# Kernel tuning notes

Hardware: AMD Instinct MI355X
Metric: run time of the kernel (lower is better)

Reference implementation:

```python
import jax, jax.numpy as jnp
import numpy as np
import math

N_HEAD = 16
N_KV_HEAD = 4
N_EMBED = 2048
HEAD_DIM = N_EMBED // N_HEAD  # 128
ROPE_BASE = 10000.0


def _rope_tables(T, dim, dtype):
    inv_freq = 1.0 / (ROPE_BASE ** (jnp.arange(0, dim, 2, dtype=jnp.float32) / dim))
    t = jnp.arange(T, dtype=jnp.float32)
    freqs = jnp.outer(t, inv_freq)            # (T, dim/2)
    emb = jnp.concatenate([freqs, freqs], -1) # (T, dim)
    return jnp.cos(emb).astype(dtype), jnp.sin(emb).astype(dtype)


def _rotate_half(x):
    half = x.shape[-1] // 2
    return jnp.concatenate([-x[..., half:], x[..., :half]], axis=-1)


def setup_inputs() -> dict:
    key = jax.random.key(0)
    kx, kq, kk, kv, ko = jax.random.split(key, 5)
    B, T, C = 2, 2048, N_EMBED
    s = 0.02
    return {
        "x": jax.random.normal(kx, (B, T, C), jnp.float32),
        "Wq": jax.random.normal(kq, (N_HEAD * HEAD_DIM, C), jnp.float32) * s,
        "Wk": jax.random.normal(kk, (N_KV_HEAD * HEAD_DIM, C), jnp.float32) * s,
        "Wv": jax.random.normal(kv, (N_KV_HEAD * HEAD_DIM, C), jnp.float32) * s,
        "Wo": jax.random.normal(ko, (C, N_HEAD * HEAD_DIM), jnp.float32) * s,
    }


def reference(x, Wq, Wk, Wv, Wo):
    B, T, C = x.shape
    H, KV, D = N_HEAD, N_KV_HEAD, HEAD_DIM
    rep = H // KV

    q = jnp.einsum('btc,oc->bto', x, Wq).reshape(B, T, H, D).transpose(0, 2, 1, 3)   # (B,H,T,D)
    k = jnp.einsum('btc,oc->bto', x, Wk).reshape(B, T, KV, D).transpose(0, 2, 1, 3)  # (B,KV,T,D)
    v = jnp.einsum('btc,oc->bto', x, Wv).reshape(B, T, KV, D).transpose(0, 2, 1, 3)

    cos, sin = _rope_tables(T, D, x.dtype)  # (T,D) broadcast over (B,h,T,D)
    q = q * cos + _rotate_half(q) * sin
    k = k * cos + _rotate_half(k) * sin

    # GQA: head h attends to kv head h // rep (== repeat_interleave in torch).
    qg = q.reshape(B, KV, rep, T, D)
    scale = 1.0 / math.sqrt(D)
    attn = jnp.einsum('bgrtd,bgsd->bgrts', qg, k) * scale  # (B,KV,rep,T,T)
    causal = jnp.tril(jnp.ones((T, T), dtype=bool))
    attn = jnp.where(causal, attn, -jnp.inf)
    attn = jax.nn.softmax(attn, axis=-1)
    out = jnp.einsum('bgrts,bgsd->bgrtd', attn, v)          # (B,KV,rep,T,D)
    out = out.reshape(B, H, T, D).transpose(0, 2, 1, 3).reshape(B, T, H * D)
    return jnp.einsum('bto,co->btc', out, Wo)
```

## Files before the change

### kernel.cpp

```cpp
#include <hip/hip_runtime.h>
#include <stdint.h>

typedef unsigned short u16;
typedef __attribute__((ext_vector_type(8))) short short8;
typedef __attribute__((ext_vector_type(4))) short short4v;
typedef __attribute__((ext_vector_type(4))) float f32x4;

#define NB_  2
#define NT_  2048
#define NC_  2048
#define NH_  16
#define NKV_ 4
#define HD_  128
#define NM_  (NB_*NT_)
#define NQKV 3072

__device__ __forceinline__ u16 f2b(float x) {
  uint32_t u = __float_as_uint(x);
  u += 0x7fffu + ((u >> 16) & 1u);
  return (u16)(u >> 16);
}
__device__ __forceinline__ float b2f(u16 x) {
  return __uint_as_float(((uint32_t)x) << 16);
}
__device__ __forceinline__ uint32_t pk2t(float a, float b) {
  return (__float_as_uint(a) >> 16) | (__float_as_uint(b) & 0xFFFF0000u);
}

typedef __attribute__((address_space(1))) uint32_t* gp1_t;
typedef __attribute__((address_space(3))) uint32_t* lp3_t;
__device__ __forceinline__ void async_ld16(const void* g, void* l) {
  __builtin_amdgcn_global_load_lds((gp1_t)(uintptr_t)g, (lp3_t)(uintptr_t)l, 16, 0, 0);
}

__global__ void f2bf_all(const float* __restrict__ x,  const float* __restrict__ wq,
                         const float* __restrict__ wk, const float* __restrict__ wv,
                         const float* __restrict__ wo,
                         u16* xb, u16* wqb, u16* wkb, u16* wvb, u16* wob,
                         float2* __restrict__ tab) {
  int bid = blockIdx.x;
  if (bid >= 18432) {
    int idx = (bid - 18432) * 256 + threadIdx.x;
    int t = idx >> 6, j = idx & 63;
    float inv = expf(-0.14391156831212787f * (float)j);
    float ang = (float)t * inv;
    tab[idx] = make_float2(cosf(ang), sinf(ang));
    return;
  }
  const float* src; u16* dst; int base;
  if      (bid < 8192)  { src = x;  dst = xb;  base = bid; }
  else if (bid < 12288) { src = wq; dst = wqb; base = bid - 8192; }
  else if (bid < 13312) { src = wk; dst = wkb; base = bid - 12288; }
  else if (bid < 14336) { src = wv; dst = wvb; base = bid - 13312; }
  else                  { src = wo; dst = wob; base = bid - 14336; }
  int i = base * 256 + threadIdx.x;
  const float4 v = ((const float4*)src)[i];
  short4v o;
  o[0] = (short)f2b(v.x); o[1] = (short)f2b(v.y);
  o[2] = (short)f2b(v.z); o[3] = (short)f2b(v.w);
  *(short4v*)(dst + (size_t)i * 4) = o;
}

__global__ void postk(const u16* __restrict__ qkv, const float2* __restrict__ tab,
                      u16* __restrict__ Qr, u16* __restrict__ Kr, u16* __restrict__ Vt) {
  __shared__ u16 tile[64][72];
  int bid = blockIdx.x;
  if (bid < 2560) {
    u16* out; int nheads; int tid; int coff; float osc;
    if (bid < 2048) { out = Qr; nheads = NH_;  tid = bid * 256 + threadIdx.x; coff = 0;
                      osc = 0.08838834764831845f; }
    else            { out = Kr; nheads = NKV_; tid = (bid - 2048) * 256 + threadIdx.x; coff = 2048;
                      osc = 1.0f; }
    int jw = tid & 7;
    int t = (tid >> 3) & (NT_ - 1);
    int bh = tid >> 14;
    int h = bh % nheads, b = bh / nheads;
    int j0 = jw * 8;
    const u16* src = qkv + ((size_t)(b * NT_ + t)) * NQKV + coff + h * HD_;
    short8 s0 = *(const short8*)(src + j0);
    short8 s1 = *(const short8*)(src + 64 + j0);
    const float4* tp = (const float4*)(tab + t * 64 + j0);
    float4 t01 = tp[0], t23 = tp[1], t45 = tp[2], t67 = tp[3];
    float cs[16] = { t01.x, t01.y, t01.z, t01.w, t23.x, t23.y, t23.z, t23.w,
                     t45.x, t45.y, t45.z, t45.w, t67.x, t67.y, t67.z, t67.w };
    short8 o0, o1;
#pragma unroll
    for (int i = 0; i < 8; ++i) {
      float q0 = b2f((u16)s0[i]), q1 = b2f((u16)s1[i]);
      float c = cs[i * 2], s = cs[i * 2 + 1];
      o0[i] = (short)f2b((q0 * c - q1 * s) * osc);
      o1[i] = (short)f2b((q1 * c + q0 * s) * osc);
    }
    u16* dst = out + ((size_t)(b * nheads + h) * NT_ + t) * HD_;
    *(short8*)(dst + j0)      = o0;
    *(short8*)(dst + 64 + j0) = o1;
  } else {
    int idx = bid - 2560;
    int tt = idx & 63, dd = idx >> 6;
    int tid = threadIdx.x;
    int r = tid >> 3, c8 = (tid & 7) * 8;
#pragma unroll
    for (int it = 0; it < 2; ++it) {
      int row = r + it * 32;
      short8 v = *(const short8*)(qkv + (size_t)(tt * 64 + row) * NQKV + 2560 + dd * 64 + c8);
      *(short8*)(&tile[row][c8]) = v;
    }
    __syncthreads();
    int b = (tt * 64) >> 11, t0 = (tt * 64) & (NT_ - 1);
    int dl = tid >> 3, t8 = (tid & 7) * 8;
#pragma unroll
    for (int it = 0; it < 2; ++it) {
      int d = dl + it * 32;
      int gcol = dd * 64 + d;
      int kv = gcol >> 7, drow = gcol & 127;
      short8 v;
#pragma unroll
      for (int k = 0; k < 8; ++k) v[k] = (short)tile[t8 + k][d];
      *(short8*)(Vt + ((size_t)(b * NKV_ + kv) * HD_ + drow) * NT_ + t0 + t8) = v;
    }
  }
}

__global__ __launch_bounds__(256, 2)
void gemm192(const u16* __restrict__ A, const u16* __restrict__ B, u16* __restrict__ C, int K)
{
  __shared__ u16 As[2 * 128 * 32];
  __shared__ u16 Bs[2 * 192 * 32];
  const int bx = blockIdx.x, by = blockIdx.y;
  const int m0 = by * 128, n0 = bx * 192;
  const int tid = threadIdx.x;
  const int wave = tid >> 6, lane = tid & 63;
  const int quad = lane >> 4, l15 = lane & 15;
  const int wm = wave >> 1, wn = wave & 1;

  const int p_local = lane >> 3;
  const int s7 = lane & 7;
  const int mlo = s7 >> 2;
  const int gg = (s7 & 3) ^ (p_local & 3);
  const int rowc = p_local * 2 + mlo;
  const int kel = gg * 8;

  const u16* Ag[2]; u16* Al[2];
#pragma unroll
  for (int q = 0; q < 2; ++q) {
    const int c = wave * 2 + q;
    Ag[q] = A + (size_t)(m0 + c * 16 + rowc) * K + kel;
    Al[q] = As + c * 512;
  }
  const u16* Bg[3]; u16* Bl[3];
#pragma unroll
  for (int q = 0; q < 3; ++q) {
    const int c = wave * 3 + q;
    Bg[q] = B + (size_t)(n0 + c * 16 + rowc) * K + kel;
    Bl[q] = Bs + c * 512;
  }

  f32x4 acc[4][6] = {};

  int a_addr[4], b_addr[6];
#pragma unroll
  for (int i = 0; i < 4; ++i) {
    int m = wm * 64 + i * 16 + l15;
    a_addr[i] = ((m >> 1) * 8 + (m & 1) * 4 + (quad ^ ((m >> 1) & 3))) * 8;
  }
#pragma unroll
  for (int i = 0; i < 6; ++i) {
    int n = wn * 96 + i * 16 + l15;
    b_addr[i] = ((n >> 1) * 8 + (n & 1) * 4 + (quad ^ ((n >> 1) & 3))) * 8;
  }

  const int nk = K >> 5;
#pragma unroll
  for (int q = 0; q < 2; ++q) async_ld16(Ag[q], Al[q]);
#pragma unroll
  for (int q = 0; q < 3; ++q) async_ld16(Bg[q], Bl[q]);

  for (int i = 0; i < nk; ++i) {
    __syncthreads();
    if (i + 1 < nk) {
      const int offA = ((i + 1) & 1) * 4096;
      const int offB = ((i + 1) & 1) * 6144;
      const int k0 = (i + 1) << 5;
#pragma unroll
      for (int q = 0; q < 2; ++q) async_ld16(Ag[q] + k0, Al[q] + offA);
#pragma unroll
      for (int q = 0; q < 3; ++q) async_ld16(Bg[q] + k0, Bl[q] + offB);
    }
    const int offA = (i & 1) * 4096;
    const int offB = (i & 1) * 6144;
    short8 af[4], bf[6];
#pragma unroll
    for (int j = 0; j < 4; ++j) af[j] = *(const short8*)(As + offA + a_addr[j]);
#pragma unroll
    for (int j = 0; j < 6; ++j) bf[j] = *(const short8*)(Bs + offB + b_addr[j]);
#pragma unroll
    for (int mb = 0; mb < 4; ++mb)
#pragma unroll
      for (int nb = 0; nb < 6; ++nb)
        acc[mb][nb] = __builtin_amdgcn_mfma_f32_16x16x32_bf16(af[mb], bf[nb], acc[mb][nb], 0, 0, 0);
  }

#pragma unroll
  for (int mb = 0; mb < 4; ++mb)
#pragma unroll
    for (int nb = 0; nb < 6; ++nb) {
      const int gn = n0 + wn * 96 + nb * 16 + l15;
#pragma unroll
      for (int r = 0; r < 4; ++r) {
        const int gm = m0 + wm * 64 + mb * 16 + quad * 4 + r;
        C[(size_t)gm * NQKV + gn] = f2b(acc[mb][nb][r]);
      }
    }
}

__global__ __launch_bounds__(256, 2)
void gemm128o(const u16* __restrict__ A, const u16* __restrict__ B, float* __restrict__ C, int K)
{
  __shared__ u16 As[2 * 128 * 32];
  __shared__ u16 Bs[2 * 128 * 32];
  const int bx = blockIdx.x, by = blockIdx.y;
  const int m0 = by * 128, n0 = bx * 128;
  const int tid = threadIdx.x;
  const int wave = tid >> 6, lane = tid & 63;
  const int quad = lane >> 4, l15 = lane & 15;
  const int wm = wave >> 1, wn = wave & 1;

  const int p_local = lane >> 3;
  const int s7 = lane & 7;
  const int mlo = s7 >> 2;
  const int gg = (s7 & 3) ^ (p_local & 3);
  const int rowc = p_local * 2 + mlo;
  const int kel = gg * 8;

  const u16* Ag[2]; const u16* Bg[2];
  u16* Al[2]; u16* Bl[2];
#pragma unroll
  for (int q = 0; q < 2; ++q) {
    const int c = wave * 2 + q;
    Ag[q] = A + (size_t)(m0 + c * 16 + rowc) * K + kel;
    Bg[q] = B + (size_t)(n0 + c * 16 + rowc) * K + kel;
    Al[q] = As + c * 512;
    Bl[q] = Bs + c * 512;
  }

  f32x4 acc[4][4] = {};

  int a_addr[4], b_addr[4];
#pragma unroll
  for (int i = 0; i < 4; ++i) {
    int m = wm * 64 + i * 16 + l15;
    a_addr[i] = ((m >> 1) * 8 + (m & 1) * 4 + (quad ^ ((m >> 1) & 3))) * 8;
    int n = wn * 64 + i * 16 + l15;
    b_addr[i] = ((n >> 1) * 8 + (n & 1) * 4 + (quad ^ ((n >> 1) & 3))) * 8;
  }

  const int nk = K >> 5;
#pragma unroll
  for (int q = 0; q < 2; ++q) {
    async_ld16(Ag[q], Al[q]);
    async_ld16(Bg[q], Bl[q]);
  }

  for (int i = 0; i < nk; ++i) {
    __syncthreads();
    if (i + 1 < nk) {
      const int off = ((i + 1) & 1) * 4096;
      const int k0 = (i + 1) << 5;
#pragma unroll
      for (int q = 0; q < 2; ++q) {
        async_ld16(Ag[q] + k0, Al[q] + off);
        async_ld16(Bg[q] + k0, Bl[q] + off);
      }
    }
    const int off = (i & 1) * 4096;
    short8 af[4], bf[4];
#pragma unroll
    for (int j = 0; j < 4; ++j) af[j] = *(const short8*)(As + off + a_addr[j]);
#pragma unroll
    for (int j = 0; j < 4; ++j) bf[j] = *(const short8*)(Bs + off + b_addr[j]);
#pragma unroll
    for (int mb = 0; mb < 4; ++mb)
#pragma unroll
      for (int nb = 0; nb < 4; ++nb)
        acc[mb][nb] = __builtin_amdgcn_mfma_f32_16x16x32_bf16(af[mb], bf[nb], acc[mb][nb], 0, 0, 0);
  }

#pragma unroll
  for (int mb = 0; mb < 4; ++mb)
#pragma unroll
    for (int nb = 0; nb < 4; ++nb) {
      const int gn = n0 + wn * 64 + nb * 16 + l15;
#pragma unroll
      for (int r = 0; r < 4; ++r) {
        const int gm = m0 + wm * 64 + mb * 16 + quad * 4 + r;
        C[(size_t)gm * NC_ + gn] = acc[mb][nb][r];
      }
    }
}

__global__ __launch_bounds__(512, 4)
void attn_kernel(const u16* __restrict__ Q, const u16* __restrict__ Kg,
                 const u16* __restrict__ Vt, u16* __restrict__ O)
{
  __shared__ u16 Ks[2 * 8192];
  __shared__ u16 Vs[2 * 8192];
  const int bx = blockIdx.x;
  const int h  = blockIdx.y;
  const int b  = blockIdx.z;
  const int qi = b ? (15 - bx) : bx;
  const int kv = h >> 2;
  const int tid = threadIdx.x;
  const int wave = tid >> 6, lane = tid & 63;
  const int quad = lane >> 4, l15 = lane & 15;
  const int qw = qi * 128 + wave * 16;

  const u16* Kbase = Kg + (size_t)(b * NKV_ + kv) * NT_ * HD_;
  const u16* Vbase = Vt + (size_t)(b * NKV_ + kv) * HD_ * NT_;

  short8 qf[4];
  {
    const u16* qb = Q + ((size_t)(b * NH_ + h) * NT_ + qw + l15) * HD_ + quad * 8;
#pragma unroll
    for (int kb = 0; kb < 4; ++kb) qf[kb] = *(const short8*)(qb + kb * 32);
  }

  const int krow = lane >> 4, kgs = lane & 15;
  const int vrow = lane >> 3, vgs = lane & 7;

  auto stage = [&](int kt, int pbuf) {
    u16* KsB = Ks + pbuf * 8192;
    u16* VsB = Vs + pbuf * 8192;
#pragma unroll
    for (int qq = 0; qq < 2; ++qq) {
      const int c = wave * 2 + qq;
      const int p  = (c >> 2) & 1;
      const int qp = c & 3;
      const int br = ((qp & 1) << 1) | (qp >> 1);
      const int kgrp = p ? (4 + (br ^ 1)) : br;
      const int srow = (c >> 3) * 32 + kgrp * 4 + krow;
      const int lrow = c * 4 + krow;
      const int gk = kgs ^ (lrow & 7);
      async_ld16(Kbase + (size_t)(kt * 64 + srow) * HD_ + gk * 8, KsB + c * 512);
      const int rv = c * 8 + vrow;
      const int gv = vgs ^ (rv & 7);
      async_ld16(Vbase + (size_t)rv * NT_ + kt * 64 + gv * 8, VsB + c * 512);
    }
  };

  const int br_q = ((quad & 1) << 1) | (quad >> 1);
  const int gt0 = br_q;
  const int gt1 = 4 + (br_q ^ 1);

  short8 vone;
#pragma unroll
  for (int j = 0; j < 8; ++j) vone[j] = (short)0x3F80;

  f32x4 acc_o[8] = {};
  f32x4 acc_l = {};
  const int nkt = 2 * qi + 2;

  stage(0, 0);

  for (int kt = 0; kt < nkt; ++kt) {
    __syncthreads();
    if (kt + 1 < nkt) stage(kt + 1, (kt + 1) & 1);
    if (kt * 64 > qw + 15) continue;

    const u16* KsB = Ks + (kt & 1) * 8192;
    const u16* VsB = Vs + (kt & 1) * 8192;

    f32x4 S[4] = {};
    __builtin_amdgcn_s_setprio(1);
#pragma unroll
    for (int nb = 0; nb < 4; ++nb) {
      const int row = nb * 16 + l15;
#pragma unroll
      for (int kb = 0; kb < 4; ++kb) {
        const int gi = kb * 4 + quad;
        short8 kfr = *(const short8*)(KsB + row * 128 + (gi ^ (row & 7)) * 8);
        S[nb] = __builtin_amdgcn_mfma_f32_16x16x32_bf16(kfr, qf[kb], S[nb], 0, 0, 0);
      }
    }
    __builtin_amdgcn_s_setprio(0);

    if (kt * 64 + 63 > qw) {
      const int qg = qw + l15;
#pragma unroll
      for (int nb = 0; nb < 4; ++nb) {
        const int kb32 = kt * 64 + (nb >> 1) * 32 + ((nb & 1) ? gt1 : gt0) * 4;
#pragma unroll
        for (int r = 0; r < 4; ++r) {
          if (kb32 + r > qg) S[nb][r] = -INFINITY;
        }
      }
    }

#pragma unroll
    for (int nb = 0; nb < 4; ++nb)
#pragma unroll
      for (int r = 0; r < 4; ++r)
        S[nb][r] = __expf(S[nb][r]);

    short8 pf[2];
    {
      uint32_t d0[4], d1[4];
#pragma unroll
      for (int nb = 0; nb < 4; ++nb) {
        d0[nb] = pk2t(S[nb][0], S[nb][1]);
        d1[nb] = pk2t(S[nb][2], S[nb][3]);
      }
      const bool hi = quad >= 2;
#pragma unroll
      for (int k2 = 0; k2 < 2; ++k2) {
        const int nbL = k2 * 2, nbH = k2 * 2 + 1;
        uint32_t own0 = hi ? d0[nbH] : d0[nbL];
        uint32_t own1 = hi ? d1[nbH] : d1[nbL];
        uint32_t c0 = (uint32_t)__shfl((int)(hi ? d0[nbL] : d0[nbH]), lane ^ 32);
        uint32_t c1 = (uint32_t)__shfl((int)(hi ? d1[nbL] : d1[nbH]), lane ^ 32);
        uint32_t w[4] = { own0, own1, c0, c1 };
        pf[k2] = *(short8*)w;
      }
    }

    acc_l = __builtin_amdgcn_mfma_f32_16x16x32_bf16(pf[0], vone, acc_l, 0, 0, 0);
    acc_l = __builtin_amdgcn_mfma_f32_16x16x32_bf16(pf[1], vone, acc_l, 0, 0, 0);

    __builtin_amdgcn_s_setprio(1);
#pragma unroll
    for (int db = 0; db < 8; ++db) {
      const int row = db * 16 + l15;
#pragma unroll
      for (int k2 = 0; k2 < 2; ++k2) {
        const int gi = k2 * 4 + quad;
        short8 vf = *(const short8*)(VsB + row * 64 + (gi ^ (row & 7)) * 8);
        acc_o[db] = __builtin_amdgcn_mfma_f32_16x16x32_bf16(pf[k2], vf, acc_o[db], 0, 0, 0);
      }
    }
    __builtin_amdgcn_s_setprio(0);
  }

  {
    float inv_r[4];
#pragma unroll
    for (int r = 0; r < 4; ++r) inv_r[r] = 1.f / acc_l[r];
    const size_t orow = ((size_t)b * NT_ + qw) * (NH_ * HD_);
#pragma unroll
    for (int db = 0; db < 8; ++db)
#pragma unroll
      for (int r = 0; r < 4; ++r)
        O[orow + (size_t)(quad * 4 + r) * (NH_ * HD_) + h * HD_ + db * 16 + l15] =
            f2b(acc_o[db][r] * inv_r[r]);
  }
}

extern "C" void kernel_launch(void* const* d_in, const int* in_sizes, int n_in,
                              void* d_out, int out_size, void* d_ws, size_t ws_size,
                              hipStream_t stream) {
  const float* x  = (const float*)d_in[0];
  const float* Wq = (const float*)d_in[1];
  const float* Wk = (const float*)d_in[2];
  const float* Wv = (const float*)d_in[3];
  const float* Wo = (const float*)d_in[4];
  float* out = (float*)d_out;
  char* ws = (char*)d_ws;
  const size_t MB = (size_t)1 << 20;
  u16* xb    = (u16*)(ws + 0);
  u16* wqkv  = (u16*)(ws + 16 * MB);
  u16* wkb   = (u16*)(ws + 24 * MB);
  u16* wvb   = (u16*)(ws + 26 * MB);
  u16* wob   = (u16*)(ws + 28 * MB);
  u16* qkvrw = (u16*)(ws + 36 * MB);
  u16* Qr    = (u16*)(ws + 60 * MB);
  u16* Kr    = (u16*)(ws + 76 * MB);
  u16* Vtb   = (u16*)(ws + 80 * MB);
  float2* tab = (float2*)(ws + 84 * MB);
  u16* Ob    = xb;

  f2bf_all<<<18944, 256, 0, stream>>>(x, Wq, Wk, Wv, Wo, xb, wqkv, wkb, wvb, wob, tab);

  gemm192<<<dim3(16, 32), 256, 0, stream>>>(xb, wqkv, qkvrw, 2048);

  postk<<<3072, 256, 0, stream>>>(qkvrw, tab, Qr, Kr, Vtb);

  attn_kernel<<<dim3(16, 16, 2), 512, 0, stream>>>(Qr, Kr, Vtb, Ob);

  gemm128o<<<dim3(16, 32), 256, 0, stream>>>(Ob, wob, out, 2048);
}
```

Before: 273.9 us.

## Halve GEMM block tiles to two waves for more blocks per GPU

The QKV and output projection GEMMs drop from 4-wave blocks with 128x192 and 128x128 tiles to 2-wave blocks with 128x96 and 128x64 tiles, and launch twice as many blocks. Each wave keeps the same per-wave MFMA tile, and the global-to-LDS loads are redistributed across the two waves through a unified pointer array. The aim is to fill the 256 CUs better, since the old grids had only 512 blocks. In exchange, A-tile reuse per block is halved, which raises global and L2 traffic.

Result: slower. 291.7 us (+6.5%).

```diff
diff --git a/kernel.cpp b/kernel.cpp
--- a/kernel.cpp
+++ b/kernel.cpp
@@ -121,17 +121,16 @@
   }
 }
 
-__global__ __launch_bounds__(256, 2)
-void gemm192(const u16* __restrict__ A, const u16* __restrict__ B, u16* __restrict__ C, int K)
+__global__ __launch_bounds__(128, 4)
+void gemm96(const u16* __restrict__ A, const u16* __restrict__ B, u16* __restrict__ C, int K)
 {
   __shared__ u16 As[2 * 128 * 32];
-  __shared__ u16 Bs[2 * 192 * 32];
+  __shared__ u16 Bs[2 * 96 * 32];
   const int bx = blockIdx.x, by = blockIdx.y;
-  const int m0 = by * 128, n0 = bx * 192;
+  const int m0 = by * 128, n0 = bx * 96;
   const int tid = threadIdx.x;
   const int wave = tid >> 6, lane = tid & 63;
   const int quad = lane >> 4, l15 = lane & 15;
-  const int wm = wave >> 1, wn = wave & 1;
 
   const int p_local = lane >> 3;
   const int s7 = lane & 7;
@@ -140,19 +139,19 @@
   const int rowc = p_local * 2 + mlo;
   const int kel = gg * 8;
 
-  const u16* Ag[2]; u16* Al[2];
-#pragma unroll
-  for (int q = 0; q < 2; ++q) {
-    const int c = wave * 2 + q;
-    Ag[q] = A + (size_t)(m0 + c * 16 + rowc) * K + kel;
-    Al[q] = As + c * 512;
-  }
-  const u16* Bg[3]; u16* Bl[3];
-#pragma unroll
-  for (int q = 0; q < 3; ++q) {
-    const int c = wave * 3 + q;
-    Bg[q] = B + (size_t)(n0 + c * 16 + rowc) * K + kel;
-    Bl[q] = Bs + c * 512;
+  const u16* Gp[7]; u16* Lp[7]; int doff[7];
+#pragma unroll
+  for (int q = 0; q < 7; ++q) {
+    const int c = wave * 7 + q;
+    if (c < 8) {
+      Gp[q] = A + (size_t)(m0 + c * 16 + rowc) * K + kel;
+      Lp[q] = As + c * 512;
+      doff[q] = 4096;
+    } else {
+      Gp[q] = B + (size_t)(n0 + (c - 8) * 16 + rowc) * K + kel;
+      Lp[q] = Bs + (c - 8) * 512;
+      doff[q] = 3072;
+    }
   }
 
   f32x4 acc[4][6] = {};
@@ -160,34 +159,29 @@
   int a_addr[4], b_addr[6];
 #pragma unroll
   for (int i = 0; i < 4; ++i) {
-    int m = wm * 64 + i * 16 + l15;
+    int m = wave * 64 + i * 16 + l15;
     a_addr[i] = ((m >> 1) * 8 + (m & 1) * 4 + (quad ^ ((m >> 1) & 3))) * 8;
   }
 #pragma unroll
   for (int i = 0; i < 6; ++i) {
-    int n = wn * 96 + i * 16 + l15;
+    int n = i * 16 + l15;
     b_addr[i] = ((n >> 1) * 8 + (n & 1) * 4 + (quad ^ ((n >> 1) & 3))) * 8;
   }
 
   const int nk = K >> 5;
 #pragma unroll
-  for (int q = 0; q < 2; ++q) async_ld16(Ag[q], Al[q]);
-#pragma unroll
-  for (int q = 0; q < 3; ++q) async_ld16(Bg[q], Bl[q]);
+  for (int q = 0; q < 7; ++q) async_ld16(Gp[q], Lp[q]);
 
   for (int i = 0; i < nk; ++i) {
     __syncthreads();
     if (i + 1 < nk) {
-      const int offA = ((i + 1) & 1) * 4096;
-      const int offB = ((i + 1) & 1) * 6144;
       const int k0 = (i + 1) << 5;
-#pragma unroll
-      for (int q = 0; q < 2; ++q) async_ld16(Ag[q] + k0, Al[q] + offA);
-#pragma unroll
-      for (int q = 0; q < 3; ++q) async_ld16(Bg[q] + k0, Bl[q] + offB);
+      const int odd = (i + 1) & 1;
+#pragma unroll
+      for (int q = 0; q < 7; ++q) async_ld16(Gp[q] + k0, Lp[q] + odd * doff[q]);
     }
     const int offA = (i & 1) * 4096;
-    const int offB = (i & 1) * 6144;
+    const int offB = (i & 1) * 3072;
     short8 af[4], bf[6];
 #pragma unroll
     for (int j = 0; j < 4; ++j) af[j] = *(const short8*)(As + offA + a_addr[j]);
@@ -204,26 +198,25 @@
   for (int mb = 0; mb < 4; ++mb)
 #pragma unroll
     for (int nb = 0; nb < 6; ++nb) {
-      const int gn = n0 + wn * 96 + nb * 16 + l15;
+      const int gn = n0 + nb * 16 + l15;
 #pragma unroll
       for (int r = 0; r < 4; ++r) {
-        const int gm = m0 + wm * 64 + mb * 16 + quad * 4 + r;
+        const int gm = m0 + wave * 64 + mb * 16 + quad * 4 + r;
         C[(size_t)gm * NQKV + gn] = f2b(acc[mb][nb][r]);
       }
     }
 }
 
-__global__ __launch_bounds__(256, 2)
-void gemm128o(const u16* __restrict__ A, const u16* __restrict__ B, float* __restrict__ C, int K)
+__global__ __launch_bounds__(128, 4)
+void gemm64o(const u16* __restrict__ A, const u16* __restrict__ B, float* __restrict__ C, int K)
 {
   __shared__ u16 As[2 * 128 * 32];
-  __shared__ u16 Bs[2 * 128 * 32];
+  __shared__ u16 Bs[2 * 64 * 32];
   const int bx = blockIdx.x, by = blockIdx.y;
-  const int m0 = by * 128, n0 = bx * 128;
+  const int m0 = by * 128, n0 = bx * 64;
   const int tid = threadIdx.x;
   const int wave = tid >> 6, lane = tid & 63;
   const int quad = lane >> 4, l15 = lane & 15;
-  const int wm = wave >> 1, wn = wave & 1;
 
   const int p_local = lane >> 3;
   const int s7 = lane & 7;
@@ -232,15 +225,19 @@
   const int rowc = p_local * 2 + mlo;
   const int kel = gg * 8;
 
-  const u16* Ag[2]; const u16* Bg[2];
-  u16* Al[2]; u16* Bl[2];
-#pragma unroll
-  for (int q = 0; q < 2; ++q) {
-    const int c = wave * 2 + q;
-    Ag[q] = A + (size_t)(m0 + c * 16 + rowc) * K + kel;
-    Bg[q] = B + (size_t)(n0 + c * 16 + rowc) * K + kel;
-    Al[q] = As + c * 512;
-    Bl[q] = Bs + c * 512;
+  const u16* Gp[6]; u16* Lp[6]; int doff[6];
+#pragma unroll
+  for (int q = 0; q < 6; ++q) {
+    const int c = wave * 6 + q;
+    if (c < 8) {
+      Gp[q] = A + (size_t)(m0 + c * 16 + rowc) * K + kel;
+      Lp[q] = As + c * 512;
+      doff[q] = 4096;
+    } else {
+      Gp[q] = B + (size_t)(n0 + (c - 8) * 16 + rowc) * K + kel;
+      Lp[q] = Bs + (c - 8) * 512;
+      doff[q] = 2048;
+    }
   }
 
   f32x4 acc[4][4] = {};
@@ -248,36 +245,31 @@
   int a_addr[4], b_addr[4];
 #pragma unroll
   for (int i = 0; i < 4; ++i) {
-    int m = wm * 64 + i * 16 + l15;
+    int m = wave * 64 + i * 16 + l15;
     a_addr[i] = ((m >> 1) * 8 + (m & 1) * 4 + (quad ^ ((m >> 1) & 3))) * 8;
-    int n = wn * 64 + i * 16 + l15;
+    int n = i * 16 + l15;
     b_addr[i] = ((n >> 1) * 8 + (n & 1) * 4 + (quad ^ ((n >> 1) & 3))) * 8;
   }
 
   const int nk = K >> 5;
 #pragma unroll
-  for (int q = 0; q < 2; ++q) {
-    async_ld16(Ag[q], Al[q]);
-    async_ld16(Bg[q], Bl[q]);
-  }
+  for (int q = 0; q < 6; ++q) async_ld16(Gp[q], Lp[q]);
 
   for (int i = 0; i < nk; ++i) {
     __syncthreads();
     if (i + 1 < nk) {
-      const int off = ((i + 1) & 1) * 4096;
       const int k0 = (i + 1) << 5;
-#pragma unroll
-      for (int q = 0; q < 2; ++q) {
-        async_ld16(Ag[q] + k0, Al[q] + off);
-        async_ld16(Bg[q] + k0, Bl[q] + off);
-      }
-    }
-    const int off = (i & 1) * 4096;
+      const int odd = (i + 1) & 1;
+#pragma unroll
+      for (int q = 0; q < 6; ++q) async_ld16(Gp[q] + k0, Lp[q] + odd * doff[q]);
+    }
+    const int offA = (i & 1) * 4096;
+    const int offB = (i & 1) * 2048;
     short8 af[4], bf[4];
 #pragma unroll
-    for (int j = 0; j < 4; ++j) af[j] = *(const short8*)(As + off + a_addr[j]);
-#pragma unroll
-    for (int j = 0; j < 4; ++j) bf[j] = *(const short8*)(Bs + off + b_addr[j]);
+    for (int j = 0; j < 4; ++j) af[j] = *(const short8*)(As + offA + a_addr[j]);
+#pragma unroll
+    for (int j = 0; j < 4; ++j) bf[j] = *(const short8*)(Bs + offB + b_addr[j]);
 #pragma unroll
     for (int mb = 0; mb < 4; ++mb)
 #pragma unroll
@@ -289,10 +281,10 @@
   for (int mb = 0; mb < 4; ++mb)
 #pragma unroll
     for (int nb = 0; nb < 4; ++nb) {
-      const int gn = n0 + wn * 64 + nb * 16 + l15;
+      const int gn = n0 + nb * 16 + l15;
 #pragma unroll
       for (int r = 0; r < 4; ++r) {
-        const int gm = m0 + wm * 64 + mb * 16 + quad * 4 + r;
+        const int gm = m0 + wave * 64 + mb * 16 + quad * 4 + r;
         C[(size_t)gm * NC_ + gn] = acc[mb][nb][r];
       }
     }
@@ -478,11 +470,11 @@
 
   f2bf_all<<<18944, 256, 0, stream>>>(x, Wq, Wk, Wv, Wo, xb, wqkv, wkb, wvb, wob, tab);
 
-  gemm192<<<dim3(16, 32), 256, 0, stream>>>(xb, wqkv, qkvrw, 2048);
+  gemm96<<<dim3(32, 32), 128, 0, stream>>>(xb, wqkv, qkvrw, 2048);
 
   postk<<<3072, 256, 0, stream>>>(qkvrw, tab, Qr, Kr, Vtb);
 
   attn_kernel<<<dim3(16, 16, 2), 512, 0, stream>>>(Qr, Kr, Vtb, Ob);
 
-  gemm128o<<<dim3(16, 32), 256, 0, stream>>>(Ob, wob, out, 2048);
-}
+  gemm64o<<<dim3(32, 32), 128, 0, stream>>>(Ob, wob, out, 2048);
+}
```
